# Optimization experiments

Hardware: AMD Instinct MI355X
Metric: run time of the kernel (lower is better)

The kernel has to match this reference:

```python
import jax, jax.numpy as jnp
import numpy as np

B, H = 16384, 1024
EPS = 1e-5


def setup_inputs() -> dict:
    key = jax.random.key(0)
    ks = jax.random.split(key, 12)
    inp = {
        "t": 0,
        "h": jax.random.normal(ks[0], (B, H), jnp.float32),
        "e": jax.random.normal(ks[1], (B, H), jnp.float32),
        # LiquidNeuron params
        "W_rec": jax.random.normal(ks[2], (H, H), jnp.float32) * 0.1,
        "bias": jnp.zeros((H,), jnp.float32),
        "tau": jnp.ones((H,), jnp.float32),
        "decay": jnp.ones((H,), jnp.float32),
        "ln_w": jnp.ones((H,), jnp.float32),
        "ln_b": jnp.zeros((H,), jnp.float32),
        # context_encoder: Linear -> ReLU -> Linear (dropout = identity in eval)
        "ce_w1": jax.random.normal(ks[3], (H, H), jnp.float32) * (1.0 / np.sqrt(H)),
        "ce_b1": jnp.zeros((H,), jnp.float32),
        "ce_w2": jax.random.normal(ks[4], (H, H), jnp.float32) * (1.0 / np.sqrt(H)),
        "ce_b2": jnp.zeros((H,), jnp.float32),
        # param_modulator
        "pm_w": jax.random.normal(ks[5], (H, H), jnp.float32) * (1.0 / np.sqrt(H)),
        "pm_b": jnp.zeros((H,), jnp.float32),
    }
    return inp


def reference(t, h, e, W_rec, bias, tau, decay, ln_w, ln_b,
              ce_w1, ce_b1, ce_w2, ce_b2, pm_w, pm_b):
    # context encoder (eval mode: dropout is identity)
    context = jnp.maximum(h @ ce_w1.T + ce_b1, 0.0) @ ce_w2.T + ce_b2  # [B,H]
    pa = context @ pm_w.T + pm_b  # param_adjustment [B,H]
    # bmm(e[:,None,:], (W_rec*(1+pa)[:,:,None]).T) == (1+pa) * (e @ W_rec.T)
    matmul_result = (1.0 + pa) * (e @ W_rec.T)  # [B,H]
    tau_adjusted = tau * jax.nn.sigmoid(pa)  # [B,H]
    dh_dt = (-decay * h + matmul_result + bias) / tau_adjusted
    # LayerNorm over last dim
    mu = jnp.mean(dh_dt, axis=-1, keepdims=True)
    var = jnp.var(dh_dt, axis=-1, keepdims=True)
    dh_dt = (dh_dt - mu) * jax.lax.rsqrt(var + EPS) * ln_w + ln_b
    return dh_dt
```

## Files before the change

kernel.cpp:

```cpp
#include <hip/hip_runtime.h>
#include <stdint.h>

#define H_DIM 1024
#define B_DIM 16384

typedef unsigned short u16;
typedef short bf16x8 __attribute__((ext_vector_type(8)));
typedef unsigned short ushort8 __attribute__((ext_vector_type(8)));
typedef float f32x4 __attribute__((ext_vector_type(4)));

__device__ __forceinline__ u16 f2bf(float f) {
  union { float f; uint32_t u; } v; v.f = f;
  uint32_t r = v.u + 0x7fffu + ((v.u >> 16) & 1u);
  return (u16)(r >> 16);
}
__device__ __forceinline__ float bf2f(u16 x) {
  union { uint32_t u; float f; } v; v.u = ((uint32_t)x) << 16;
  return v.f;
}

#define GLDS16(gsrc, ldst)                                                                 \
  __builtin_amdgcn_global_load_lds((const __attribute__((address_space(1))) void*)(gsrc),  \
                                   (__attribute__((address_space(3))) void*)(ldst), 16, 0, 0)

__global__ __launch_bounds__(256) void cvt_all(const float* __restrict__ h,
                                               const float* __restrict__ e,
                                               const float* __restrict__ w0f,
                                               const float* __restrict__ w1f,
                                               const float* __restrict__ w2f,
                                               const float* __restrict__ w3f,
                                               u16* __restrict__ hb, u16* __restrict__ eb,
                                               u16* __restrict__ o0, u16* __restrict__ o1,
                                               u16* __restrict__ o2, u16* __restrict__ o3,
                                               const float* __restrict__ tau,
                                               float* __restrict__ rtau) {
  const int b = blockIdx.x;
  if (b >= 5120) {
    for (int i = threadIdx.x; i < H_DIM; i += 256) rtau[i] = 1.0f / tau[i];
    return;
  }
  if (b < 4096) {
    const float4* in4 = (const float4*)(b < 2048 ? h : e);
    ushort4* out4 = (ushort4*)(b < 2048 ? hb : eb);
    const int base = (b & 2047) * 256 + threadIdx.x;
#pragma unroll
    for (int g = 0; g < 2; ++g) {
      float4 v[4];
#pragma unroll
      for (int u = 0; u < 4; ++u) v[u] = in4[base + (g * 4 + u) * 524288];
#pragma unroll
      for (int u = 0; u < 4; ++u) {
        ushort4 o;
        o.x = f2bf(v[u].x); o.y = f2bf(v[u].y); o.z = f2bf(v[u].z); o.w = f2bf(v[u].w);
        out4[base + (g * 4 + u) * 524288] = o;
      }
    }
  } else {
    const int which = (b - 4096) >> 8;
    const float4* in4 =
        (const float4*)(which == 0 ? w0f : which == 1 ? w1f : which == 2 ? w2f : w3f);
    ushort4* out4 = (ushort4*)(which == 0 ? o0 : which == 1 ? o1 : which == 2 ? o2 : o3);
    const int base = ((b - 4096) & 255) * 256 + threadIdx.x;
    float4 v[4];
#pragma unroll
    for (int u = 0; u < 4; ++u) v[u] = in4[base + u * 65536];
#pragma unroll
    for (int u = 0; u < 4; ++u) {
      ushort4 o;
      o.x = f2bf(v[u].x); o.y = f2bf(v[u].y); o.z = f2bf(v[u].z); o.w = f2bf(v[u].w);
      out4[base + u * 65536] = o;
    }
  }
}

template <int MODE>
__device__ __forceinline__ void subtile_step(u16* shp, int slot, int slot3, int aoff, int boff,
                                             int wv, const u16*& pA0, const u16*& pA1,
                                             const u16*& pB0, const u16*& pB1,
                                             f32x4 (&acc)[8][4]) {
  const u16* Ab = shp + slot * 16384 + aoff;
  const u16* Bb = shp + slot * 16384 + 8192 + boff;
  bf16x8 aF[8], bF[4];
#pragma unroll
  for (int i = 0; i < 4; ++i) aF[i] = *(const bf16x8*)(Ab + i * 512);
#pragma unroll
  for (int i = 0; i < 4; ++i) bF[i] = *(const bf16x8*)(Bb + i * 512);
#pragma unroll
  for (int i = 4; i < 8; ++i) aF[i] = *(const bf16x8*)(Ab + i * 512);
  if (MODE == 3) {
    u16* da = shp + slot3 * 16384 + wv * 1024;
    GLDS16(pA0, da); GLDS16(pA1, da + 512);
    u16* db = shp + slot3 * 16384 + 8192 + wv * 1024;
    GLDS16(pB0, db); GLDS16(pB1, db + 512);
    pA0 += 32; pA1 += 32; pB0 += 32; pB1 += 32;
  }
  __builtin_amdgcn_s_setprio(1);
#pragma unroll
  for (int mf = 0; mf < 4; ++mf)
#pragma unroll
    for (int nf = 0; nf < 4; ++nf)
      acc[mf][nf] = __builtin_amdgcn_mfma_f32_16x16x32_bf16(aF[mf], bF[nf], acc[mf][nf], 0, 0, 0);
#pragma unroll
  for (int mf = 4; mf < 8; ++mf)
#pragma unroll
    for (int nf = 0; nf < 4; ++nf)
      acc[mf][nf] = __builtin_amdgcn_mfma_f32_16x16x32_bf16(aF[mf], bF[nf], acc[mf][nf], 0, 0, 0);
  __builtin_amdgcn_s_setprio(0);
  if (MODE == 3) asm volatile("s_waitcnt vmcnt(8)" ::: "memory");
  if (MODE == 2) asm volatile("s_waitcnt vmcnt(4)" ::: "memory");
  if (MODE == 1) asm volatile("s_waitcnt vmcnt(0)" ::: "memory");
  __builtin_amdgcn_s_barrier();
}

template <bool RELU, bool HASBIAS, typename OUT>
__global__ __launch_bounds__(512, 2) void gemm256(const u16* __restrict__ A,
                                                  const u16* __restrict__ W,
                                                  const float* __restrict__ bias,
                                                  OUT* __restrict__ C) {
  extern __shared__ u16 sh[];
  const int t = threadIdx.x;
  const int wv = t >> 6, l = t & 63;
  const int wm = wv >> 2, wn = wv & 3;
  const int l15 = l & 15, lg = l >> 4;

  const int bid = blockIdx.x;
  const int logical = (bid & 7) * 32 + (bid >> 3);
  const int m0 = (logical >> 2) * 256;
  const int n0 = (logical & 3) * 256;

  const int koff = (lg ^ ((l15 >> 1) & 3)) * 8;
  const int aoff = (wm * 128 + l15) * 32 + koff;
  const int boff = (wn * 64 + l15) * 32 + koff;

  const int rowst = wv * 32 + (l >> 2);
  const int ksl = ((l & 3) ^ ((l >> 3) & 3)) * 8;
  const u16* pA0 = A + (size_t)(m0 + rowst) * H_DIM + ksl;
  const u16* pA1 = pA0 + 16 * H_DIM;
  const u16* pB0 = W + (size_t)(n0 + rowst) * H_DIM + ksl;
  const u16* pB1 = pB0 + 16 * H_DIM;

  f32x4 acc[8][4] = {};

#pragma unroll
  for (int s = 0; s < 3; ++s) {
    u16* da = sh + s * 16384 + wv * 1024;
    GLDS16(pA0, da); GLDS16(pA1, da + 512);
    u16* db = sh + s * 16384 + 8192 + wv * 1024;
    GLDS16(pB0, db); GLDS16(pB1, db + 512);
    pA0 += 32; pA1 += 32; pB0 += 32; pB1 += 32;
  }
  asm volatile("s_waitcnt vmcnt(8)" ::: "memory");
  __builtin_amdgcn_s_barrier();

  for (int s = 0; s < 29; ++s)
    subtile_step<3>(sh, s & 3, (s + 3) & 3, aoff, boff, wv, pA0, pA1, pB0, pB1, acc);
  subtile_step<2>(sh, 1, 0, aoff, boff, wv, pA0, pA1, pB0, pB1, acc);
  subtile_step<1>(sh, 2, 0, aoff, boff, wv, pA0, pA1, pB0, pB1, acc);
  subtile_step<0>(sh, 3, 0, aoff, boff, wv, pA0, pA1, pB0, pB1, acc);

  float bv[4];
#pragma unroll
  for (int nf = 0; nf < 4; ++nf)
    bv[nf] = HASBIAS ? bias[n0 + wn * 64 + nf * 16 + l15] : 0.0f;
#pragma unroll
  for (int mf = 0; mf < 8; ++mf) {
#pragma unroll
    for (int nf = 0; nf < 4; ++nf) {
      const int col = n0 + wn * 64 + nf * 16 + l15;
#pragma unroll
      for (int j = 0; j < 4; ++j) {
        const int row = m0 + wm * 128 + mf * 16 + lg * 4 + j;
        float v = acc[mf][nf][j] + bv[nf];
        if (RELU) v = fmaxf(v, 0.0f);
        if constexpr (sizeof(OUT) == 2)
          C[(size_t)row * H_DIM + col] = (OUT)f2bf(v);
        else
          C[(size_t)row * H_DIM + col] = v;
      }
    }
  }
}

__global__ __launch_bounds__(256) void liquid_ln(const u16* __restrict__ hb,
                                                 const u16* __restrict__ pa,
                                                 const u16* __restrict__ ev,
                                                 const float* __restrict__ bias,
                                                 const float* __restrict__ rtau,
                                                 const float* __restrict__ decay,
                                                 const float* __restrict__ lnw,
                                                 const float* __restrict__ lnb,
                                                 float* __restrict__ out) {
  const int wv = threadIdx.x >> 6, l = threadIdx.x & 63;
  const int row = blockIdx.x * 4 + wv;
  const size_t rb = (size_t)row * H_DIM;

  float d[16];
  float s = 0.f, ss = 0.f;
#pragma unroll
  for (int c = 0; c < 2; ++c) {
    const int col = c * 512 + l * 8;
    float b8[8], r8[8], dc8[8];
    *(float4*)b8 = *(const float4*)(bias + col);
    *(float4*)(b8 + 4) = *(const float4*)(bias + col + 4);
    *(float4*)r8 = *(const float4*)(rtau + col);
    *(float4*)(r8 + 4) = *(const float4*)(rtau + col + 4);
    *(float4*)dc8 = *(const float4*)(decay + col);
    *(float4*)(dc8 + 4) = *(const float4*)(decay + col + 4);
    ushort8 hv = *(const ushort8*)(hb + rb + col);
    ushort8 pv = *(const ushort8*)(pa + rb + col);
    ushort8 evv = *(const ushort8*)(ev + rb + col);
#pragma unroll
    for (int j = 0; j < 8; ++j) {
      const float hf = bf2f(hv[j]);
      const float p = bf2f(pv[j]);
      const float e = bf2f(evv[j]);
      const float num = fmaf(-dc8[j], hf, fmaf(1.0f + p, e, b8[j]));
      const float val = num * (1.0f + __expf(-p)) * r8[j];
      d[c * 8 + j] = val;
      s += val;
      ss += val * val;
    }
  }
#pragma unroll
  for (int off = 32; off; off >>= 1) {
    s += __shfl_xor(s, off);
    ss += __shfl_xor(ss, off);
  }
  const float mu = s * (1.0f / H_DIM);
  const float var = ss * (1.0f / H_DIM) - mu * mu;
  const float rstd = rsqrtf(var + 1e-5f);

#pragma unroll
  for (int c = 0; c < 2; ++c) {
    const int col = c * 512 + l * 8;
    float w8[8], lb8[8], o[8];
    *(float4*)w8 = *(const float4*)(lnw + col);
    *(float4*)(w8 + 4) = *(const float4*)(lnw + col + 4);
    *(float4*)lb8 = *(const float4*)(lnb + col);
    *(float4*)(lb8 + 4) = *(const float4*)(lnb + col + 4);
#pragma unroll
    for (int j = 0; j < 8; ++j) o[j] = fmaf((d[c * 8 + j] - mu) * rstd, w8[j], lb8[j]);
    *(float4*)(out + rb + col) = *(float4*)o;
    *(float4*)(out + rb + col + 4) = *(float4*)(o + 4);
  }
}

extern "C" void kernel_launch(void* const* d_in, const int* in_sizes, int n_in,
                              void* d_out, int out_size, void* d_ws, size_t ws_size,
                              hipStream_t stream) {
  const float* h = (const float*)d_in[1];
  const float* e = (const float*)d_in[2];
  const float* Wrec = (const float*)d_in[3];
  const float* bias = (const float*)d_in[4];
  const float* tau = (const float*)d_in[5];
  const float* decay = (const float*)d_in[6];
  const float* lnw = (const float*)d_in[7];
  const float* lnb = (const float*)d_in[8];
  const float* ce_w1 = (const float*)d_in[9];
  const float* ce_b1 = (const float*)d_in[10];
  const float* ce_w2 = (const float*)d_in[11];
  const float* ce_b2 = (const float*)d_in[12];
  const float* pm_w = (const float*)d_in[13];
  const float* pm_b = (const float*)d_in[14];
  float* out = (float*)d_out;

  char* ws = (char*)d_ws;
  const size_t MB = 1024 * 1024;
  u16* w1b = (u16*)(ws + 0 * MB);
  u16* w2b = (u16*)(ws + 2 * MB);
  u16* w3b = (u16*)(ws + 4 * MB);
  u16* w4b = (u16*)(ws + 6 * MB);
  u16* hbf = (u16*)(ws + 8 * MB);
  u16* ebf = (u16*)(ws + 40 * MB);
  u16* t1 = (u16*)(ws + 72 * MB);
  u16* ctx = (u16*)(ws + 104 * MB);
  u16* pab = (u16*)(ws + 72 * MB);
  u16* evb = (u16*)(ws + 104 * MB);
  float* rtau = (float*)(ws + 136 * MB);

  cvt_all<<<5121, 256, 0, stream>>>(h, e, ce_w1, ce_w2, pm_w, Wrec, hbf, ebf, w1b, w2b, w3b, w4b,
                                    tau, rtau);

  const int LDS_BYTES = 131072;
  hipFuncSetAttribute((const void*)gemm256<true, true, u16>,
                      hipFuncAttributeMaxDynamicSharedMemorySize, LDS_BYTES);
  hipFuncSetAttribute((const void*)gemm256<false, true, u16>,
                      hipFuncAttributeMaxDynamicSharedMemorySize, LDS_BYTES);
  hipFuncSetAttribute((const void*)gemm256<false, false, u16>,
                      hipFuncAttributeMaxDynamicSharedMemorySize, LDS_BYTES);

  const int NWG = (B_DIM / 256) * (H_DIM / 256);
  gemm256<true, true, u16><<<NWG, 512, LDS_BYTES, stream>>>(hbf, w1b, ce_b1, t1);
  gemm256<false, true, u16><<<NWG, 512, LDS_BYTES, stream>>>(t1, w2b, ce_b2, ctx);
  gemm256<false, true, u16><<<NWG, 512, LDS_BYTES, stream>>>(ctx, w3b, pm_b, pab);
  gemm256<false, false, u16><<<NWG, 512, LDS_BYTES, stream>>>(ebf, w4b, nullptr, evb);

  liquid_ln<<<B_DIM / 4, 256, 0, stream>>>(hbf, pab, evb, bias, rtau, decay, lnw, lnb, out);
}
```

Baseline: 215.3 us.

## Fold context-encoder second linear into param modulator via precomputed weight product

Because there is no nonlinearity between ce_w2 and pm_w, the two linears are merged: W32 = pm_w @ ce_w2 and b32 = pm_w @ ce_b2 + pm_b are computed once per call with small kernels (a transpose-convert of ce_w2, a bias matvec, and a 1024^3 MFMA GEMM). This removes one full 16384x1024x1024 GEMM and its intermediate activation traffic. The weight conversion kernel is also rewritten to use contiguous 8-element groups. The cost is extra small launches and an additional bf16 rounding of the combined weight, which changes numerics slightly.

```diff
diff --git a/kernel.cpp b/kernel.cpp
--- a/kernel.cpp
+++ b/kernel.cpp
@@ -23,54 +23,131 @@
   __builtin_amdgcn_global_load_lds((const __attribute__((address_space(1))) void*)(gsrc),  \
                                    (__attribute__((address_space(3))) void*)(ldst), 16, 0, 0)
 
+__device__ __forceinline__ void cvt_region(const float* __restrict__ in, u16* __restrict__ out,
+                                           int tid, int nthr, int ngroups) {
+  const float4* in4 = (const float4*)in;
+  ushort8* out8 = (ushort8*)out;
+  for (int gi = tid; gi < ngroups; gi += nthr) {
+    float4 a = in4[2 * gi];
+    float4 b = in4[2 * gi + 1];
+    ushort8 o;
+    o[0] = f2bf(a.x); o[1] = f2bf(a.y); o[2] = f2bf(a.z); o[3] = f2bf(a.w);
+    o[4] = f2bf(b.x); o[5] = f2bf(b.y); o[6] = f2bf(b.z); o[7] = f2bf(b.w);
+    out8[gi] = o;
+  }
+}
+
 __global__ __launch_bounds__(256) void cvt_all(const float* __restrict__ h,
                                                const float* __restrict__ e,
-                                               const float* __restrict__ w0f,
                                                const float* __restrict__ w1f,
-                                               const float* __restrict__ w2f,
-                                               const float* __restrict__ w3f,
+                                               const float* __restrict__ pmwf,
+                                               const float* __restrict__ wrecf,
                                                u16* __restrict__ hb, u16* __restrict__ eb,
-                                               u16* __restrict__ o0, u16* __restrict__ o1,
-                                               u16* __restrict__ o2, u16* __restrict__ o3,
+                                               u16* __restrict__ o1, u16* __restrict__ o3,
+                                               u16* __restrict__ o4,
                                                const float* __restrict__ tau,
                                                float* __restrict__ rtau) {
   const int b = blockIdx.x;
-  if (b >= 5120) {
+  const int BH8 = (B_DIM * H_DIM) / 8;
+  const int HH8 = (H_DIM * H_DIM) / 8;
+  if (b < 2048) {
+    cvt_region(h, hb, b * 256 + threadIdx.x, 2048 * 256, BH8);
+  } else if (b < 4096) {
+    cvt_region(e, eb, (b - 2048) * 256 + threadIdx.x, 2048 * 256, BH8);
+  } else if (b < 4352) {
+    cvt_region(w1f, o1, (b - 4096) * 256 + threadIdx.x, 256 * 256, HH8);
+  } else if (b < 4608) {
+    cvt_region(pmwf, o3, (b - 4352) * 256 + threadIdx.x, 256 * 256, HH8);
+  } else if (b < 4864) {
+    cvt_region(wrecf, o4, (b - 4608) * 256 + threadIdx.x, 256 * 256, HH8);
+  } else {
     for (int i = threadIdx.x; i < H_DIM; i += 256) rtau[i] = 1.0f / tau[i];
-    return;
-  }
-  if (b < 4096) {
-    const float4* in4 = (const float4*)(b < 2048 ? h : e);
-    ushort4* out4 = (ushort4*)(b < 2048 ? hb : eb);
-    const int base = (b & 2047) * 256 + threadIdx.x;
-#pragma unroll
-    for (int g = 0; g < 2; ++g) {
-      float4 v[4];
-#pragma unroll
-      for (int u = 0; u < 4; ++u) v[u] = in4[base + (g * 4 + u) * 524288];
-#pragma unroll
-      for (int u = 0; u < 4; ++u) {
-        ushort4 o;
-        o.x = f2bf(v[u].x); o.y = f2bf(v[u].y); o.z = f2bf(v[u].z); o.w = f2bf(v[u].w);
-        out4[base + (g * 4 + u) * 524288] = o;
+  }
+}
+
+__global__ __launch_bounds__(256) void tr_cvt_w2(const float* __restrict__ in,
+                                                 u16* __restrict__ out) {
+  __shared__ float tile[64][65];
+  const int t = threadIdx.x;
+  const int r0 = (blockIdx.x >> 4) * 64;
+  const int c0 = (blockIdx.x & 15) * 64;
+  const float4* in4 = (const float4*)in;
+#pragma unroll
+  for (int it = 0; it < 4; ++it) {
+    const int idx = it * 256 + t;
+    const int r = idx >> 4, c4 = idx & 15;
+    float4 v = in4[(size_t)(r0 + r) * 256 + (c0 >> 2) + c4];
+    tile[r][c4 * 4 + 0] = v.x; tile[r][c4 * 4 + 1] = v.y;
+    tile[r][c4 * 4 + 2] = v.z; tile[r][c4 * 4 + 3] = v.w;
+  }
+  __syncthreads();
+  ushort4* out4 = (ushort4*)out;
+#pragma unroll
+  for (int it = 0; it < 4; ++it) {
+    const int idx = it * 256 + t;
+    const int c = idx >> 4, r4 = idx & 15;
+    ushort4 o;
+    o.x = f2bf(tile[r4 * 4 + 0][c]); o.y = f2bf(tile[r4 * 4 + 1][c]);
+    o.z = f2bf(tile[r4 * 4 + 2][c]); o.w = f2bf(tile[r4 * 4 + 3][c]);
+    out4[(size_t)(c0 + c) * 256 + (r0 >> 2) + r4] = o;
+  }
+}
+
+__global__ __launch_bounds__(256) void b32_prep(const float* __restrict__ pmw,
+                                                const float* __restrict__ ceb2,
+                                                const float* __restrict__ pmb,
+                                                float* __restrict__ b32) {
+  const int i = blockIdx.x * 256 + threadIdx.x;
+  const float4* w4 = (const float4*)(pmw + (size_t)i * H_DIM);
+  const float4* b4 = (const float4*)ceb2;
+  float acc = pmb[i];
+  for (int k = 0; k < 256; ++k) {
+    float4 w = w4[k], b = b4[k];
+    acc += w.x * b.x + w.y * b.y + w.z * b.z + w.w * b.w;
+  }
+  b32[i] = acc;
+}
+
+__global__ __launch_bounds__(256) void w32_gemm(const u16* __restrict__ A,
+                                                const u16* __restrict__ Wt,
+                                                u16* __restrict__ C) {
+  const int t = threadIdx.x;
+  const int wv = t >> 6, l = t & 63;
+  const int l15 = l & 15, lg = l >> 4;
+  const int m0 = (blockIdx.x >> 4) * 64 + (wv >> 1) * 32;
+  const int n0 = (blockIdx.x & 15) * 64 + (wv & 1) * 32;
+
+  const u16* ap0 = A + (size_t)(m0 + l15) * H_DIM + lg * 8;
+  const u16* ap1 = ap0 + 16 * H_DIM;
+  const u16* bp0 = Wt + (size_t)(n0 + l15) * H_DIM + lg * 8;
+  const u16* bp1 = bp0 + 16 * H_DIM;
+
+  f32x4 acc[2][2] = {};
+#pragma unroll
+  for (int kt = 0; kt < 32; ++kt) {
+    bf16x8 aF[2], bF[2];
+    aF[0] = *(const bf16x8*)(ap0 + kt * 32);
+    aF[1] = *(const bf16x8*)(ap1 + kt * 32);
+    bF[0] = *(const bf16x8*)(bp0 + kt * 32);
+    bF[1] = *(const bf16x8*)(bp1 + kt * 32);
+#pragma unroll
+    for (int mi = 0; mi < 2; ++mi)
+#pragma unroll
+      for (int ni = 0; ni < 2; ++ni)
+        acc[mi][ni] =
+            __builtin_amdgcn_mfma_f32_16x16x32_bf16(aF[mi], bF[ni], acc[mi][ni], 0, 0, 0);
+  }
+#pragma unroll
+  for (int mi = 0; mi < 2; ++mi)
+#pragma unroll
+    for (int ni = 0; ni < 2; ++ni) {
+      const int col = n0 + ni * 16 + l15;
+#pragma unroll
+      for (int j = 0; j < 4; ++j) {
+        const int row = m0 + mi * 16 + lg * 4 + j;
+        C[(size_t)row * H_DIM + col] = f2bf(acc[mi][ni][j]);
       }
     }
-  } else {
-    const int which = (b - 4096) >> 8;
-    const float4* in4 =
-        (const float4*)(which == 0 ? w0f : which == 1 ? w1f : which == 2 ? w2f : w3f);
-    ushort4* out4 = (ushort4*)(which == 0 ? o0 : which == 1 ? o1 : which == 2 ? o2 : o3);
-    const int base = ((b - 4096) & 255) * 256 + threadIdx.x;
-    float4 v[4];
-#pragma unroll
-    for (int u = 0; u < 4; ++u) v[u] = in4[base + u * 65536];
-#pragma unroll
-    for (int u = 0; u < 4; ++u) {
-      ushort4 o;
-      o.x = f2bf(v[u].x); o.y = f2bf(v[u].y); o.z = f2bf(v[u].z); o.w = f2bf(v[u].w);
-      out4[base + u * 65536] = o;
-    }
-  }
 }
 
 template <int MODE>
@@ -267,19 +344,22 @@
   char* ws = (char*)d_ws;
   const size_t MB = 1024 * 1024;
   u16* w1b = (u16*)(ws + 0 * MB);
-  u16* w2b = (u16*)(ws + 2 * MB);
+  u16* w2t = (u16*)(ws + 2 * MB);
   u16* w3b = (u16*)(ws + 4 * MB);
   u16* w4b = (u16*)(ws + 6 * MB);
-  u16* hbf = (u16*)(ws + 8 * MB);
-  u16* ebf = (u16*)(ws + 40 * MB);
-  u16* t1 = (u16*)(ws + 72 * MB);
-  u16* ctx = (u16*)(ws + 104 * MB);
-  u16* pab = (u16*)(ws + 72 * MB);
-  u16* evb = (u16*)(ws + 104 * MB);
-  float* rtau = (float*)(ws + 136 * MB);
-
-  cvt_all<<<5121, 256, 0, stream>>>(h, e, ce_w1, ce_w2, pm_w, Wrec, hbf, ebf, w1b, w2b, w3b, w4b,
-                                    tau, rtau);
+  u16* W32b = (u16*)(ws + 8 * MB);
+  float* rtau = (float*)(ws + 10 * MB);
+  float* b32 = (float*)(ws + 10 * MB + 8192);
+  u16* hbf = (u16*)(ws + 12 * MB);
+  u16* ebf = (u16*)(ws + 44 * MB);
+  u16* t1 = (u16*)(ws + 76 * MB);
+  u16* evb = (u16*)(ws + 76 * MB);
+  u16* pab = (u16*)(ws + 108 * MB);
+
+  cvt_all<<<4865, 256, 0, stream>>>(h, e, ce_w1, pm_w, Wrec, hbf, ebf, w1b, w3b, w4b, tau, rtau);
+  tr_cvt_w2<<<256, 256, 0, stream>>>(ce_w2, w2t);
+  b32_prep<<<4, 256, 0, stream>>>(pm_w, ce_b2, pm_b, b32);
+  w32_gemm<<<256, 256, 0, stream>>>(w3b, w2t, W32b);
 
   const int LDS_BYTES = 131072;
   hipFuncSetAttribute((const void*)gemm256<true, true, u16>,
@@ -291,8 +371,7 @@
 
   const int NWG = (B_DIM / 256) * (H_DIM / 256);
   gemm256<true, true, u16><<<NWG, 512, LDS_BYTES, stream>>>(hbf, w1b, ce_b1, t1);
-  gemm256<false, true, u16><<<NWG, 512, LDS_BYTES, stream>>>(t1, w2b, ce_b2, ctx);
-  gemm256<false, true, u16><<<NWG, 512, LDS_BYTES, stream>>>(ctx, w3b, pm_b, pab);
+  gemm256<false, true, u16><<<NWG, 512, LDS_BYTES, stream>>>(t1, W32b, b32, pab);
   gemm256<false, false, u16><<<NWG, 512, LDS_BYTES, stream>>>(ebf, w4b, nullptr, evb);
 
   liquid_ln<<<B_DIM / 4, 256, 0, stream>>>(hbf, pab, evb, bias, rtau, decay, lnw, lnb, out);
```

New measurement: 222.5 us. +3.3%, slower.
